# Kernel tuning notes

Hardware: AMD Instinct MI355X
Metric: run time of the kernel (lower is better)

The kernel has to match this reference:

```python
import math
import jax, jax.numpy as jnp
import numpy as np

T, D, H = 2048, 1024, 16
DH = D // H
DFF = 4 * D
EPS = 1e-5


def gelu(x):
    c = math.sqrt(2.0 / math.pi)
    return 0.5 * x * (1.0 + jnp.tanh(c * (x + 0.044715 * jnp.power(x, 3))))


def layer_norm(x, w, b):
    mu = jnp.mean(x, axis=-1, keepdims=True)
    var = jnp.var(x, axis=-1, keepdims=True)
    return (x - mu) / jnp.sqrt(var + EPS) * w + b


def setup_inputs() -> dict:
    key = jax.random.key(0)
    ks = jax.random.split(key, 8)
    s = lambda fan_in: 1.0 / math.sqrt(fan_in)
    return {
        "x": jax.random.normal(ks[0], (T, D), jnp.float32),
        "w_kqv": jax.random.uniform(ks[1], (3 * D, D), jnp.float32, -s(D), s(D)),
        "b_kqv": jnp.zeros((3 * D,), jnp.float32),
        "w_o": jax.random.uniform(ks[2], (D, D), jnp.float32, -s(D), s(D)),
        "b_o": jnp.zeros((D,), jnp.float32),
        "ln1_w": jnp.ones((D,), jnp.float32),
        "ln1_b": jnp.zeros((D,), jnp.float32),
        "ln2_w": jnp.ones((D,), jnp.float32),
        "ln2_b": jnp.zeros((D,), jnp.float32),
        "w_up": jax.random.uniform(ks[3], (DFF, D), jnp.float32, -s(D), s(D)),
        "b_up": jnp.zeros((DFF,), jnp.float32),
        "w_down": jax.random.uniform(ks[4], (D, DFF), jnp.float32, -s(DFF), s(DFF)),
        "b_down": jnp.zeros((D,), jnp.float32),
    }


def _block(x, w_kqv, b_kqv, w_o, b_o, ln1_w, ln1_b, ln2_w, ln2_b,
           w_up, b_up, w_down, b_down):
    t = x.shape[0]
    # --- causal attention ---
    h = layer_norm(x, ln1_w, ln1_b)
    kqv = h @ w_kqv.T + b_kqv                      # [t, 3D]
    k, q, v = jnp.split(kqv, 3, axis=-1)
    # rearrange 't (d h) -> h t d' : head index is the FAST axis (as in source)
    to_heads = lambda m: m.reshape(t, DH, H).transpose(2, 0, 1)  # [H, t, DH]
    k, q, v = to_heads(k), to_heads(q), to_heads(v)
    # NOTE: source divides by sqrt(1/d) == multiplies by sqrt(d_head)
    logits = jnp.einsum('hqd,hkd->hqk', q, k) * math.sqrt(DH)
    mask = jnp.tril(jnp.ones((t, t), dtype=bool))
    logits = jnp.where(mask, logits, -jnp.inf)
    attn_w = jax.nn.softmax(logits, axis=-1)       # [H, t, t]
    hv = jnp.einsum('hqK,hKd->hqd', attn_w, v)     # [H, t, DH]
    # rearrange 'h q d -> q (h d)' : head index is the SLOW axis (as in source)
    hv = hv.transpose(1, 0, 2).reshape(t, D)
    x = x + (hv @ w_o.T + b_o)
    # --- MLP ---
    h2 = layer_norm(x, ln2_w, ln2_b)
    z = gelu(h2 @ w_up.T + b_up) @ w_down.T + b_down
    return x + z


def reference(x, w_kqv, b_kqv, w_o, b_o, ln1_w, ln1_b, ln2_w, ln2_b,
              w_up, b_up, w_down, b_down):
    return _block(x, w_kqv, b_kqv, w_o, b_o, ln1_w, ln1_b, ln2_w, ln2_b,
                  w_up, b_up, w_down, b_down)
```

## Files before the change

### kernel.cpp

```cpp
#include <hip/hip_runtime.h>
#include <math.h>

#define TT 2048
#define DD 1024
#define NH 16
#define DHD 64
#define DFF 4096

typedef __attribute__((ext_vector_type(8))) short short8;
typedef __attribute__((ext_vector_type(4))) float f32x4;

#define MFMA16(a, b, c) __builtin_amdgcn_mfma_f32_16x16x32_bf16(a, b, c, 0, 0, 0)
#define GLDS16(gp, lp) __builtin_amdgcn_global_load_lds( \
    (const __attribute__((address_space(1))) void*)(gp), \
    (__attribute__((address_space(3))) void*)(lp), 16, 0, 0)

static __device__ __forceinline__ unsigned short f2b(float f) {
  unsigned u = __builtin_bit_cast(unsigned, f);
  u = u + 0x7fffu + ((u >> 16) & 1u);
  return (unsigned short)(u >> 16);
}
static __device__ __forceinline__ float b2f(unsigned short b) {
  return __builtin_bit_cast(float, (unsigned)b << 16);
}

__global__ __launch_bounds__(256) void f2b4_kernel(const float* __restrict__ s0,
    const float* __restrict__ s1, const float* __restrict__ s2,
    const float* __restrict__ s3, unsigned short* __restrict__ out) {
  int i = blockIdx.x * 256 + threadIdx.x;
  float4 v;
  if (i < 786432) {
    int row = i >> 8, kk = i & 255;
    int sec = row >> 10, wi = row & 1023;
    int src = (sec << 10) + ((wi & 63) << 4) + (wi >> 6);
    v = ((const float4*)s0)[(src << 8) + kk];
  } else if (i < 1048576) {
    v = ((const float4*)s1)[i - 786432];
  } else if (i < 2097152) {
    v = ((const float4*)s2)[i - 1048576];
  } else {
    v = ((const float4*)s3)[i - 2097152];
  }
  ushort4 o;
  o.x = f2b(v.x); o.y = f2b(v.y); o.z = f2b(v.z); o.w = f2b(v.w);
  ((ushort4*)out)[i] = o;
}

__global__ __launch_bounds__(256) void ln_kernel(const float* __restrict__ x,
    const float* __restrict__ w, const float* __restrict__ b,
    unsigned short* __restrict__ out) {
  int row = blockIdx.x;
  const float4* xr = (const float4*)(x + (size_t)row * DD);
  float4 v = xr[threadIdx.x];
  float s  = v.x + v.y + v.z + v.w;
  float ss = v.x * v.x + v.y * v.y + v.z * v.z + v.w * v.w;
  for (int o = 32; o > 0; o >>= 1) {
    s  += __shfl_down(s, o);
    ss += __shfl_down(ss, o);
  }
  __shared__ float red[10];
  int lane = threadIdx.x & 63, wv = threadIdx.x >> 6;
  if (lane == 0) { red[wv] = s; red[4 + wv] = ss; }
  __syncthreads();
  if (threadIdx.x == 0) {
    float S  = red[0] + red[1] + red[2] + red[3];
    float SS = red[4] + red[5] + red[6] + red[7];
    float mu  = S * (1.0f / DD);
    float var = SS * (1.0f / DD) - mu * mu;
    red[8] = mu;
    red[9] = rsqrtf(var + 1e-5f);
  }
  __syncthreads();
  float mu = red[8], inv = red[9];
  float4 wv4 = ((const float4*)w)[threadIdx.x];
  float4 bv4 = ((const float4*)b)[threadIdx.x];
  ushort4 o4;
  o4.x = f2b((v.x - mu) * inv * wv4.x + bv4.x);
  o4.y = f2b((v.y - mu) * inv * wv4.y + bv4.y);
  o4.z = f2b((v.z - mu) * inv * wv4.z + bv4.z);
  o4.w = f2b((v.w - mu) * inv * wv4.w + bv4.w);
  ((ushort4*)(out + (size_t)row * DD))[threadIdx.x] = o4;
}

__global__ __launch_bounds__(256, 4) void gemm6(
    const unsigned short* __restrict__ A,
    const unsigned short* __restrict__ Bw,
    unsigned short* __restrict__ Cp,
    unsigned short* __restrict__ Cp2,
    int M, int N, int K, int KS, int CX, int CY, int SPLITA) {
  __shared__ char lds[32768];
  const int tid = threadIdx.x;
  const int w = tid >> 6, l = tid & 63;
  const int l15 = l & 15, lhi = l >> 4;

  const int GX = N >> 7, GYM = M >> 7;
  const int xcd = blockIdx.x & 7, s = blockIdx.x >> 3;
  const int ncx = GX / CX;
  const int bx = (xcd % ncx) * CX + (s % CX);
  const int yz = (xcd / ncx) * CY + (s / CX);
  const int by = yz % GYM, bz = yz / GYM;

  const int row0 = by << 7, col0 = bx << 7;
  const int kbeg = bz * KS;
  const int wm = (w >> 1) * 64, wn = (w & 1) * 64;

  f32x4 acc[4][4] = {};

  const int srow = w * 32 + (l >> 2);
  const int scol = (l & 3) * 16;
  const char* aS = (const char*)A + ((size_t)(row0 + srow) * K + kbeg) * 2 + scol;
  const char* bS = (const char*)Bw + ((size_t)(col0 + srow) * K + kbeg) * 2 + scol;
  const size_t r16 = (size_t)K * 32;
  const int aO = w * 2048, bO = 8192 + w * 2048;
  const int NT = KS >> 5;

  auto STAGE = [&](int t) {
    char* base = lds + (t & 1) * 16384;
    const char* a = aS + (size_t)t * 64;
    const char* b = bS + (size_t)t * 64;
    GLDS16(a,       base + aO);
    GLDS16(a + r16, base + aO + 1024);
    GLDS16(b,       base + bO);
    GLDS16(b + r16, base + bO + 1024);
  };
  auto COMPUTE = [&](int t) {
    const char* Ab = lds + (t & 1) * 16384;
    const char* Bb = Ab + 8192;
    short8 af[4], bf[4];
#pragma unroll
    for (int mi = 0; mi < 4; ++mi)
      af[mi] = *(const short8*)(Ab + (wm + mi * 16 + l15) * 64 + lhi * 16);
#pragma unroll
    for (int ni = 0; ni < 4; ++ni)
      bf[ni] = *(const short8*)(Bb + (wn + ni * 16 + l15) * 64 + lhi * 16);
    __builtin_amdgcn_s_setprio(1);
#pragma unroll
    for (int mi = 0; mi < 4; ++mi)
#pragma unroll
      for (int ni = 0; ni < 4; ++ni)
        acc[mi][ni] = MFMA16(af[mi], bf[ni], acc[mi][ni]);
    __builtin_amdgcn_s_setprio(0);
  };

  STAGE(0);
  for (int t = 0; t < NT; ++t) {
    if (t + 1 < NT) STAGE(t + 1);
    __builtin_amdgcn_sched_barrier(0);
    if (t + 1 < NT) asm volatile("s_waitcnt vmcnt(4)" ::: "memory");
    else            asm volatile("s_waitcnt vmcnt(0)" ::: "memory");
    __builtin_amdgcn_s_barrier();
    __builtin_amdgcn_sched_barrier(0);
    COMPUTE(t);
    __builtin_amdgcn_sched_barrier(0);
    __builtin_amdgcn_s_barrier();
  }

  unsigned short* base;
  size_t off;
  if (bz < SPLITA) { base = Cp;  off = (size_t)bz * M * N; }
  else             { base = Cp2; off = (size_t)(bz - SPLITA) * M * N; }
#pragma unroll
  for (int mi = 0; mi < 4; ++mi)
#pragma unroll
    for (int r = 0; r < 4; ++r) {
      size_t row = (size_t)(row0 + wm + mi * 16 + lhi * 4 + r);
#pragma unroll
      for (int ni = 0; ni < 4; ++ni)
        base[off + row * N + col0 + wn + ni * 16 + l15] = f2b(acc[mi][ni][r]);
    }
}

template<int MODE>
__global__ __launch_bounds__(256) void reduce2b(const unsigned short* __restrict__ p0,
    const unsigned short* __restrict__ p1, const float* __restrict__ bias,
    unsigned short* __restrict__ out, int n4) {
  int i = blockIdx.x * 256 + threadIdx.x;
  ushort4 a = ((const ushort4*)p0)[i];
  ushort4 b = ((const ushort4*)p1)[i];
  float4 bb = ((const float4*)bias)[i % n4];
  float v0 = b2f(a.x) + b2f(b.x) + bb.x;
  float v1 = b2f(a.y) + b2f(b.y) + bb.y;
  float v2 = b2f(a.z) + b2f(b.z) + bb.z;
  float v3 = b2f(a.w) + b2f(b.w) + bb.w;
  if (MODE == 1) {
    const float c = 0.7978845608028654f;
    v0 = 0.5f * v0 * (1.0f + tanhf(c * (v0 + 0.044715f * v0 * v0 * v0)));
    v1 = 0.5f * v1 * (1.0f + tanhf(c * (v1 + 0.044715f * v1 * v1 * v1)));
    v2 = 0.5f * v2 * (1.0f + tanhf(c * (v2 + 0.044715f * v2 * v2 * v2)));
    v3 = 0.5f * v3 * (1.0f + tanhf(c * (v3 + 0.044715f * v3 * v3 * v3)));
  }
  if (MODE == 2) {
    int c4 = i % 768;
    if (c4 >= 256 && c4 < 512) { v0 *= 8.f; v1 *= 8.f; v2 *= 8.f; v3 *= 8.f; }
  }
  ushort4 o;
  o.x = f2b(v0); o.y = f2b(v1); o.z = f2b(v2); o.w = f2b(v3);
  ((ushort4*)out)[i] = o;
}

__global__ __launch_bounds__(256) void reduce4_ln(const unsigned short* __restrict__ p,
    const float* __restrict__ bias, const float* __restrict__ resid,
    const float* __restrict__ lnw, const float* __restrict__ lnb,
    float* __restrict__ x2, unsigned short* __restrict__ hout) {
  int row = blockIdx.x;
  int i = row * 256 + threadIdx.x;
  float4 r = ((const float4*)resid)[i];
  float4 bb = ((const float4*)bias)[threadIdx.x];
  float o0 = r.x + bb.x, o1 = r.y + bb.y, o2 = r.z + bb.z, o3 = r.w + bb.w;
#pragma unroll
  for (int z = 0; z < 4; ++z) {
    ushort4 pv = ((const ushort4*)(p + (size_t)z * TT * DD))[i];
    o0 += b2f(pv.x); o1 += b2f(pv.y); o2 += b2f(pv.z); o3 += b2f(pv.w);
  }
  float4 o; o.x = o0; o.y = o1; o.z = o2; o.w = o3;
  ((float4*)x2)[i] = o;
  float s  = o0 + o1 + o2 + o3;
  float ss = o0 * o0 + o1 * o1 + o2 * o2 + o3 * o3;
  for (int of = 32; of > 0; of >>= 1) {
    s  += __shfl_down(s, of);
    ss += __shfl_down(ss, of);
  }
  __shared__ float red[10];
  int lane = threadIdx.x & 63, wv = threadIdx.x >> 6;
  if (lane == 0) { red[wv] = s; red[4 + wv] = ss; }
  __syncthreads();
  if (threadIdx.x == 0) {
    float S  = red[0] + red[1] + red[2] + red[3];
    float SS = red[4] + red[5] + red[6] + red[7];
    float mu  = S * (1.0f / DD);
    float var = SS * (1.0f / DD) - mu * mu;
    red[8] = mu;
    red[9] = rsqrtf(var + 1e-5f);
  }
  __syncthreads();
  float mu = red[8], inv = red[9];
  float4 wv4 = ((const float4*)lnw)[threadIdx.x];
  float4 bv4 = ((const float4*)lnb)[threadIdx.x];
  ushort4 o4;
  o4.x = f2b((o0 - mu) * inv * wv4.x + bv4.x);
  o4.y = f2b((o1 - mu) * inv * wv4.y + bv4.y);
  o4.z = f2b((o2 - mu) * inv * wv4.z + bv4.z);
  o4.w = f2b((o3 - mu) * inv * wv4.w + bv4.w);
  ((ushort4*)(hout + (size_t)row * DD))[threadIdx.x] = o4;
}

__global__ __launch_bounds__(256) void reduce8(const unsigned short* __restrict__ pA,
    const unsigned short* __restrict__ pB, const float* __restrict__ bias,
    const float* __restrict__ resid, float* __restrict__ out) {
  int i = blockIdx.x * 256 + threadIdx.x;
  float4 r = ((const float4*)resid)[i];
  float4 bb = ((const float4*)bias)[i & (DD / 4 - 1)];
  float o0 = r.x + bb.x, o1 = r.y + bb.y, o2 = r.z + bb.z, o3 = r.w + bb.w;
#pragma unroll
  for (int z = 0; z < 4; ++z) {
    ushort4 pv = ((const ushort4*)(pA + (size_t)z * TT * DD))[i];
    o0 += b2f(pv.x); o1 += b2f(pv.y); o2 += b2f(pv.z); o3 += b2f(pv.w);
    ushort4 qv = ((const ushort4*)(pB + (size_t)z * TT * DD))[i];
    o0 += b2f(qv.x); o1 += b2f(qv.y); o2 += b2f(qv.z); o3 += b2f(qv.w);
  }
  float4 o; o.x = o0; o.y = o1; o.z = o2; o.w = o3;
  ((float4*)out)[i] = o;
}

__global__ __launch_bounds__(256) void transpose_v(const unsigned short* __restrict__ kqz,
    unsigned short* __restrict__ Vt) {
  const int h = blockIdx.y;
  const int t0 = blockIdx.x * 64;
  __shared__ unsigned short Vs[64][65];
  for (int idx = threadIdx.x; idx < 4096; idx += 256) {
    int t = idx >> 6, d = idx & 63;
    Vs[t][d] = kqz[(size_t)(t0 + t) * (3 * DD) + 2 * DD + h * 64 + d];
  }
  __syncthreads();
  for (int idx = threadIdx.x; idx < 4096; idx += 256) {
    int d = idx >> 6, t = idx & 63;
    Vt[(size_t)(h * DHD + d) * TT + t0 + t] = Vs[t][d];
  }
}

__global__ __launch_bounds__(256) void attn5(
    const unsigned short* __restrict__ kqz,
    const unsigned short* __restrict__ Vt,
    unsigned short* __restrict__ hvp,
    float2* __restrict__ mlarr) {
  const int bid = blockIdx.x;
  const int xcd = bid & 7, s = bid >> 3;
  const int half = s & 1;
  const int j = s >> 1;
  const int hs = j & 1;
  const int qb = 31 - (j >> 1);
  const int h  = xcd * 2 + hs;
  const int q0 = qb * 64;
  const int NT = (qb + 2) >> 1;
  const int t0 = half ? (NT + 1) >> 1 : 0;
  const int t1 = half ? NT : (NT + 1) >> 1;

  const int tid = threadIdx.x;
  const int w = tid >> 6, l = tid & 63;
  const int l15 = l & 15, lhi = l >> 4;

  unsigned short* hvO = hvp + (size_t)half * TT * DD;
  float2* mlO = mlarr + (size_t)(half * NH + h) * TT;

  if (t0 >= t1) {
#pragma unroll
    for (int r = 0; r < 4; ++r) {
      size_t orow = (size_t)(q0 + w * 16 + lhi * 4 + r) * DD + h * 64;
#pragma unroll
      for (int dt = 0; dt < 4; ++dt) hvO[orow + dt * 16 + l15] = 0;
    }
    if (lhi == 0) mlO[q0 + w * 16 + l15] = make_float2(-1e30f, 0.0f);
    return;
  }

  __shared__ char lds[81920];
  char* Ps = lds + 65536 + w * 4096;

  const char* kqzB = (const char*)kqz;
  const char* VhB  = (const char*)(Vt + (size_t)h * DHD * TT);
  const size_t KROW = 3 * DD * 2;
  const size_t VROW = TT * 2;

  const unsigned short* Qb = kqz + (size_t)(q0 + w * 16 + l15) * (3 * DD) + DD + h * 64;
  short8 qf0 = *(const short8*)(Qb + lhi * 8);
  short8 qf1 = *(const short8*)(Qb + 32 + lhi * 8);

  f32x4 oacc[4] = {};
  float m = -1e30f, lsum = 0.0f;

  const int kr8 = l >> 3;
  const int kcolb = ((l & 7) * 16) ^ (kr8 << 4);
  const int vg = l >> 4;
  const int vbase = (l & 15) * 16;
  const int kswz = (l15 & 7) << 4;
  const int vpswz = (l15 & 15) << 4;

  auto stageKV = [&](int kt2) {
    const int buf = kt2 & 1;
    const int k0n = kt2 * 128;
    char* kb = lds + buf * 16384 + w * 4096;
    const char* ks = kqzB + (size_t)(k0n + w * 32 + kr8) * KROW + h * 128 + kcolb;
    GLDS16(ks,             kb);
    GLDS16(ks +  8 * KROW, kb + 1024);
    GLDS16(ks + 16 * KROW, kb + 2048);
    GLDS16(ks + 24 * KROW, kb + 3072);
    char* vb = lds + 32768 + buf * 16384 + w * 4096;
    const char* vs = VhB + (size_t)(w * 16 + vg) * VROW + (size_t)k0n * 2;
    GLDS16(vs +             (vbase ^ ((vg +  0) << 4)), vb);
    GLDS16(vs +  4 * VROW + (vbase ^ ((vg +  4) << 4)), vb + 1024);
    GLDS16(vs +  8 * VROW + (vbase ^ ((vg +  8) << 4)), vb + 2048);
    GLDS16(vs + 12 * VROW + (vbase ^ ((vg + 12) << 4)), vb + 3072);
  };

  stageKV(t0);
  if (t0 + 1 < t1) stageKV(t0 + 1);

  for (int kt = t0; kt < t1; ++kt) {
    const int k0 = kt * 128;
    __builtin_amdgcn_sched_barrier(0);
    if (kt + 1 < t1) asm volatile("s_waitcnt vmcnt(8)" ::: "memory");
    else             asm volatile("s_waitcnt vmcnt(0)" ::: "memory");
    __builtin_amdgcn_s_barrier();
    __builtin_amdgcn_sched_barrier(0);

    const char* Kb = lds + (kt & 1) * 16384;
    const char* Vb = lds + 32768 + (kt & 1) * 16384;

    f32x4 sacc[8] = {};
    __builtin_amdgcn_s_setprio(1);
#pragma unroll
    for (int nt = 0; nt < 8; ++nt) {
      const char* rp = Kb + (nt * 16 + l15) * 128;
      short8 kb0 = *(const short8*)(rp + ((lhi * 16) ^ kswz));
      short8 kb1 = *(const short8*)(rp + ((64 + lhi * 16) ^ kswz));
      sacc[nt] = MFMA16(kb0, qf0, sacc[nt]);
      sacc[nt] = MFMA16(kb1, qf1, sacc[nt]);
    }
    __builtin_amdgcn_s_setprio(0);

    if (kt == NT - 1) {
      const int qq = q0 + w * 16 + l15;
#pragma unroll
      for (int nt = 0; nt < 8; ++nt)
#pragma unroll
        for (int r = 0; r < 4; ++r)
          if (k0 + nt * 16 + lhi * 4 + r > qq) sacc[nt][r] = -1e30f;
    }

    float tmax = -1e30f;
#pragma unroll
    for (int nt = 0; nt < 8; ++nt)
#pragma unroll
      for (int r = 0; r < 4; ++r) tmax = fmaxf(tmax, sacc[nt][r]);
    tmax = fmaxf(tmax, __shfl_xor(tmax, 16));
    tmax = fmaxf(tmax, __shfl_xor(tmax, 32));
    float mnew = fmaxf(m, tmax);
    float al = __expf(m - mnew);
    m = mnew;
    float ssum = 0.0f;
#pragma unroll
    for (int nt = 0; nt < 8; ++nt)
#pragma unroll
      for (int r = 0; r < 4; ++r) {
        float p = __expf(sacc[nt][r] - mnew);
        sacc[nt][r] = p;
        ssum += p;
      }
    ssum += __shfl_xor(ssum, 16);
    ssum += __shfl_xor(ssum, 32);
    lsum = lsum * al + ssum;

    {
      char* pp = Ps + l15 * 256;
#pragma unroll
      for (int nt = 0; nt < 8; ++nt) {
        uint2 pk;
        pk.x = (unsigned)f2b(sacc[nt][0]) | ((unsigned)f2b(sacc[nt][1]) << 16);
        pk.y = (unsigned)f2b(sacc[nt][2]) | ((unsigned)f2b(sacc[nt][3]) << 16);
        *(uint2*)(pp + ((nt * 32 + lhi * 8) ^ vpswz)) = pk;
      }
    }

    float alr[4];
#pragma unroll
    for (int r = 0; r < 4; ++r) alr[r] = __shfl(al, (l & 48) | (lhi * 4 + r));
#pragma unroll
    for (int dt = 0; dt < 4; ++dt)
#pragma unroll
      for (int r = 0; r < 4; ++r) oacc[dt][r] *= alr[r];

    const char* pr = Ps + l15 * 256;
    short8 pa[4];
#pragma unroll
    for (int kc = 0; kc < 4; ++kc)
      pa[kc] = *(const short8*)(pr + ((kc * 64 + lhi * 16) ^ vpswz));
    __builtin_amdgcn_s_setprio(1);
#pragma unroll
    for (int dt = 0; dt < 4; ++dt) {
      const char* vr = Vb + (dt * 16 + l15) * 256;
#pragma unroll
      for (int kc = 0; kc < 4; ++kc) {
        short8 vbf = *(const short8*)(vr + ((kc * 64 + lhi * 16) ^ vpswz));
        oacc[dt] = MFMA16(pa[kc], vbf, oacc[dt]);
      }
    }
    __builtin_amdgcn_s_setprio(0);

    __builtin_amdgcn_sched_barrier(0);
    __builtin_amdgcn_s_barrier();
    if (kt + 2 < t1) stageKV(kt + 2);
  }

  float lr4[4];
#pragma unroll
  for (int r = 0; r < 4; ++r) {
    float lv = __shfl(lsum, (l & 48) | (lhi * 4 + r));
    lr4[r] = 1.0f / lv;
  }
#pragma unroll
  for (int r = 0; r < 4; ++r) {
    size_t orow = (size_t)(q0 + w * 16 + lhi * 4 + r) * DD + h * 64;
#pragma unroll
    for (int dt = 0; dt < 4; ++dt)
      hvO[orow + dt * 16 + l15] = f2b(oacc[dt][r] * lr4[r]);
  }
  if (lhi == 0) mlO[q0 + w * 16 + l15] = make_float2(m, lsum);
}

__global__ __launch_bounds__(256) void merge_attn(
    const unsigned short* __restrict__ hvp, const float2* __restrict__ mlarr,
    unsigned short* __restrict__ hv) {
  int row = blockIdx.x;
  int t = threadIdx.x;
  int h = t >> 4;
  float2 ml0 = mlarr[(size_t)h * TT + row];
  float2 ml1 = mlarr[(size_t)(NH + h) * TT + row];
  float M = fmaxf(ml0.x, ml1.x);
  float w0 = ml0.y * __expf(ml0.x - M);
  float w1 = ml1.y * __expf(ml1.x - M);
  float inv = 1.0f / (w0 + w1);
  w0 *= inv; w1 *= inv;
  size_t i = (size_t)row * 256 + t;
  ushort4 a = ((const ushort4*)hvp)[i];
  ushort4 b = ((const ushort4*)(hvp + (size_t)TT * DD))[i];
  ushort4 o;
  o.x = f2b(w0 * b2f(a.x) + w1 * b2f(b.x));
  o.y = f2b(w0 * b2f(a.y) + w1 * b2f(b.y));
  o.z = f2b(w0 * b2f(a.z) + w1 * b2f(b.z));
  o.w = f2b(w0 * b2f(a.w) + w1 * b2f(b.w));
  ((ushort4*)hv)[i] = o;
}

extern "C" void kernel_launch(void* const* d_in, const int* in_sizes, int n_in,
                              void* d_out, int out_size, void* d_ws, size_t ws_size,
                              hipStream_t stream) {
  const float* x     = (const float*)d_in[0];
  const float* w_kqv = (const float*)d_in[1];
  const float* b_kqv = (const float*)d_in[2];
  const float* w_o   = (const float*)d_in[3];
  const float* b_o   = (const float*)d_in[4];
  const float* ln1_w = (const float*)d_in[5];
  const float* ln1_b = (const float*)d_in[6];
  const float* ln2_w = (const float*)d_in[7];
  const float* ln2_b = (const float*)d_in[8];
  const float* w_up  = (const float*)d_in[9];
  const float* b_up  = (const float*)d_in[10];
  const float* w_dn  = (const float*)d_in[11];
  const float* b_dn  = (const float*)d_in[12];
  float* out = (float*)d_out;

  char* W = (char*)d_ws;
  unsigned short* wkqv_b = (unsigned short*)(W);
  unsigned short* wo_b   = (unsigned short*)(W + 6291456);
  unsigned short* wup_b  = (unsigned short*)(W + 8388608);
  unsigned short* wdn_b  = (unsigned short*)(W + 16777216);
  unsigned short* h_b    = (unsigned short*)(W + 25165824);
  float2*         mlarr  = (float2*)(W + 25165824);
  unsigned short* rA     = (unsigned short*)(W + 29360128);
  unsigned short* rB     = (unsigned short*)(W + 46137344);
  unsigned short* hvhalf = (unsigned short*)(W + 46137344);
  unsigned short* Vtg    = (unsigned short*)(W + 54525952);
  unsigned short* hv_b   = (unsigned short*)(W + 58720256);
  float*          x2     = (float*)(W + 62914560);
  unsigned short* pB2    = (unsigned short*)(W);

  f2b4_kernel<<<3145728 / 256, 256, 0, stream>>>(w_kqv, w_o, w_up, w_dn, wkqv_b);

  ln_kernel<<<TT, 256, 0, stream>>>(x, ln1_w, ln1_b, h_b);
  gemm6<<<768, 256, 0, stream>>>(h_b, wkqv_b, rA, rB,
      TT, 3 * DD, DD, DD / 2, 3, 32, 1);
  reduce2b<2><<<TT * 3 * DD / 4 / 256, 256, 0, stream>>>(
      rA, rB, b_kqv, rA, 3 * DD / 4);
  transpose_v<<<dim3(TT / 64, NH), 256, 0, stream>>>(rA, Vtg);
  attn5<<<1024, 256, 0, stream>>>(rA, Vtg, hvhalf, mlarr);
  merge_attn<<<TT, 256, 0, stream>>>(hvhalf, mlarr, hv_b);
  gemm6<<<512, 256, 0, stream>>>(hv_b, wo_b, rA, rA,
      TT, DD, DD, DD / 4, 1, 64, 4);
  reduce4_ln<<<TT, 256, 0, stream>>>(rA, b_o, x, ln2_w, ln2_b, x2, h_b);
  gemm6<<<1024, 256, 0, stream>>>(h_b, wup_b, rA, rB,
      TT, DFF, DD, DD / 2, 4, 32, 1);
  reduce2b<1><<<TT * DFF / 4 / 256, 256, 0, stream>>>(
      rA, rB, b_up, rA, DFF / 4);
  gemm6<<<1024, 256, 0, stream>>>(rA, wdn_b, rB, pB2,
      TT, DD, DFF, DFF / 8, 1, 128, 4);
  reduce8<<<TT * DD / 4 / 256, 256, 0, stream>>>(rB, pB2, b_dn, x2, out);
}
```

Measured before the change: 186.7 us.

## Split attention KV range into four chunks with single-buffered LDS

```diff
diff --git a/kernel.cpp b/kernel.cpp
--- a/kernel.cpp
+++ b/kernel.cpp
@@ -278,29 +278,30 @@
   }
 }
 
-__global__ __launch_bounds__(256) void attn5(
+__global__ __launch_bounds__(256) void attn6(
     const unsigned short* __restrict__ kqz,
     const unsigned short* __restrict__ Vt,
-    unsigned short* __restrict__ hvp,
+    unsigned short* __restrict__ hvA,
+    unsigned short* __restrict__ hvB,
     float2* __restrict__ mlarr) {
   const int bid = blockIdx.x;
   const int xcd = bid & 7, s = bid >> 3;
-  const int half = s & 1;
-  const int j = s >> 1;
+  const int quarter = s & 3;
+  const int j = s >> 2;
   const int hs = j & 1;
   const int qb = 31 - (j >> 1);
   const int h  = xcd * 2 + hs;
   const int q0 = qb * 64;
   const int NT = (qb + 2) >> 1;
-  const int t0 = half ? (NT + 1) >> 1 : 0;
-  const int t1 = half ? NT : (NT + 1) >> 1;
+  const int t0 = (quarter * NT) >> 2;
+  const int t1 = ((quarter + 1) * NT) >> 2;
 
   const int tid = threadIdx.x;
   const int w = tid >> 6, l = tid & 63;
   const int l15 = l & 15, lhi = l >> 4;
 
-  unsigned short* hvO = hvp + (size_t)half * TT * DD;
-  float2* mlO = mlarr + (size_t)(half * NH + h) * TT;
+  unsigned short* hvO = ((quarter & 2) ? hvB : hvA) + (size_t)(quarter & 1) * TT * DD;
+  float2* mlO = mlarr + (size_t)(quarter * NH + h) * TT;
 
   if (t0 >= t1) {
 #pragma unroll
@@ -313,8 +314,8 @@
     return;
   }
 
-  __shared__ char lds[81920];
-  char* Ps = lds + 65536 + w * 4096;
+  __shared__ char lds[49152];
+  char* Ps = lds + 32768 + w * 4096;
 
   const char* kqzB = (const char*)kqz;
   const char* VhB  = (const char*)(Vt + (size_t)h * DHD * TT);
@@ -336,15 +337,14 @@
   const int vpswz = (l15 & 15) << 4;
 
   auto stageKV = [&](int kt2) {
-    const int buf = kt2 & 1;
     const int k0n = kt2 * 128;
-    char* kb = lds + buf * 16384 + w * 4096;
+    char* kb = lds + w * 4096;
     const char* ks = kqzB + (size_t)(k0n + w * 32 + kr8) * KROW + h * 128 + kcolb;
     GLDS16(ks,             kb);
     GLDS16(ks +  8 * KROW, kb + 1024);
     GLDS16(ks + 16 * KROW, kb + 2048);
     GLDS16(ks + 24 * KROW, kb + 3072);
-    char* vb = lds + 32768 + buf * 16384 + w * 4096;
+    char* vb = lds + 16384 + w * 4096;
     const char* vs = VhB + (size_t)(w * 16 + vg) * VROW + (size_t)k0n * 2;
     GLDS16(vs +             (vbase ^ ((vg +  0) << 4)), vb);
     GLDS16(vs +  4 * VROW + (vbase ^ ((vg +  4) << 4)), vb + 1024);
@@ -352,19 +352,16 @@
     GLDS16(vs + 12 * VROW + (vbase ^ ((vg + 12) << 4)), vb + 3072);
   };
 
-  stageKV(t0);
-  if (t0 + 1 < t1) stageKV(t0 + 1);
-
   for (int kt = t0; kt < t1; ++kt) {
     const int k0 = kt * 128;
+    stageKV(kt);
     __builtin_amdgcn_sched_barrier(0);
-    if (kt + 1 < t1) asm volatile("s_waitcnt vmcnt(8)" ::: "memory");
-    else             asm volatile("s_waitcnt vmcnt(0)" ::: "memory");
+    asm volatile("s_waitcnt vmcnt(0)" ::: "memory");
     __builtin_amdgcn_s_barrier();
     __builtin_amdgcn_sched_barrier(0);
 
-    const char* Kb = lds + (kt & 1) * 16384;
-    const char* Vb = lds + 32768 + (kt & 1) * 16384;
+    const char* Kb = lds;
+    const char* Vb = lds + 16384;
 
     f32x4 sacc[8] = {};
     __builtin_amdgcn_s_setprio(1);
@@ -448,7 +445,6 @@
 
     __builtin_amdgcn_sched_barrier(0);
     __builtin_amdgcn_s_barrier();
-    if (kt + 2 < t1) stageKV(kt + 2);
   }
 
   float lr4[4];
@@ -467,27 +463,33 @@
   if (lhi == 0) mlO[q0 + w * 16 + l15] = make_float2(m, lsum);
 }
 
-__global__ __launch_bounds__(256) void merge_attn(
-    const unsigned short* __restrict__ hvp, const float2* __restrict__ mlarr,
-    unsigned short* __restrict__ hv) {
+__global__ __launch_bounds__(256) void merge_attn4(
+    const unsigned short* __restrict__ hvA, const unsigned short* __restrict__ hvB,
+    const float2* __restrict__ mlarr, unsigned short* __restrict__ hv) {
   int row = blockIdx.x;
   int t = threadIdx.x;
   int h = t >> 4;
-  float2 ml0 = mlarr[(size_t)h * TT + row];
-  float2 ml1 = mlarr[(size_t)(NH + h) * TT + row];
-  float M = fmaxf(ml0.x, ml1.x);
+  float2 ml0 = mlarr[(size_t)(0 * NH + h) * TT + row];
+  float2 ml1 = mlarr[(size_t)(1 * NH + h) * TT + row];
+  float2 ml2 = mlarr[(size_t)(2 * NH + h) * TT + row];
+  float2 ml3 = mlarr[(size_t)(3 * NH + h) * TT + row];
+  float M = fmaxf(fmaxf(ml0.x, ml1.x), fmaxf(ml2.x, ml3.x));
   float w0 = ml0.y * __expf(ml0.x - M);
   float w1 = ml1.y * __expf(ml1.x - M);
-  float inv = 1.0f / (w0 + w1);
-  w0 *= inv; w1 *= inv;
+  float w2 = ml2.y * __expf(ml2.x - M);
+  float w3 = ml3.y * __expf(ml3.x - M);
+  float inv = 1.0f / (w0 + w1 + w2 + w3);
+  w0 *= inv; w1 *= inv; w2 *= inv; w3 *= inv;
   size_t i = (size_t)row * 256 + t;
-  ushort4 a = ((const ushort4*)hvp)[i];
-  ushort4 b = ((const ushort4*)(hvp + (size_t)TT * DD))[i];
+  ushort4 a = ((const ushort4*)hvA)[i];
+  ushort4 b = ((const ushort4*)(hvA + (size_t)TT * DD))[i];
+  ushort4 c = ((const ushort4*)hvB)[i];
+  ushort4 d = ((const ushort4*)(hvB + (size_t)TT * DD))[i];
   ushort4 o;
-  o.x = f2b(w0 * b2f(a.x) + w1 * b2f(b.x));
-  o.y = f2b(w0 * b2f(a.y) + w1 * b2f(b.y));
-  o.z = f2b(w0 * b2f(a.z) + w1 * b2f(b.z));
-  o.w = f2b(w0 * b2f(a.w) + w1 * b2f(b.w));
+  o.x = f2b(w0 * b2f(a.x) + w1 * b2f(b.x) + w2 * b2f(c.x) + w3 * b2f(d.x));
+  o.y = f2b(w0 * b2f(a.y) + w1 * b2f(b.y) + w2 * b2f(c.y) + w3 * b2f(d.y));
+  o.z = f2b(w0 * b2f(a.z) + w1 * b2f(b.z) + w2 * b2f(c.z) + w3 * b2f(d.z));
+  o.w = f2b(w0 * b2f(a.w) + w1 * b2f(b.w) + w2 * b2f(c.w) + w3 * b2f(d.w));
   ((ushort4*)hv)[i] = o;
 }
 
@@ -518,10 +520,11 @@
   float2*         mlarr  = (float2*)(W + 25165824);
   unsigned short* rA     = (unsigned short*)(W + 29360128);
   unsigned short* rB     = (unsigned short*)(W + 46137344);
-  unsigned short* hvhalf = (unsigned short*)(W + 46137344);
+  unsigned short* hvq01  = (unsigned short*)(W + 46137344);
   unsigned short* Vtg    = (unsigned short*)(W + 54525952);
   unsigned short* hv_b   = (unsigned short*)(W + 58720256);
   float*          x2     = (float*)(W + 62914560);
+  unsigned short* hvq23  = (unsigned short*)(W + 62914560);
   unsigned short* pB2    = (unsigned short*)(W);
 
   f2b4_kernel<<<3145728 / 256, 256, 0, stream>>>(w_kqv, w_o, w_up, w_dn, wkqv_b);
@@ -532,8 +535,8 @@
   reduce2b<2><<<TT * 3 * DD / 4 / 256, 256, 0, stream>>>(
       rA, rB, b_kqv, rA, 3 * DD / 4);
   transpose_v<<<dim3(TT / 64, NH), 256, 0, stream>>>(rA, Vtg);
-  attn5<<<1024, 256, 0, stream>>>(rA, Vtg, hvhalf, mlarr);
-  merge_attn<<<TT, 256, 0, stream>>>(hvhalf, mlarr, hv_b);
+  attn6<<<2048, 256, 0, stream>>>(rA, Vtg, hvq01, hvq23, mlarr);
+  merge_attn4<<<TT, 256, 0, stream>>>(hvq01, hvq23, mlarr, hv_b);
   gemm6<<<512, 256, 0, stream>>>(hv_b, wo_b, rA, rA,
       TT, DD, DD, DD / 4, 1, 64, 4);
   reduce4_ln<<<TT, 256, 0, stream>>>(rA, b_o, x, ln2_w, ln2_b, x2, h_b);
```

New measurement: 189.5 us. Within noise of the previous version (+1.5%).
